# Optimization experiments

Measured on AMD Instinct MI355X. Metric: run time of the kernel, lower is better.

Reference implementation:

```python
import jax, jax.numpy as jnp
import numpy as np

B = 128        # graphs
NPG = 64       # nodes per graph (num_node)
N = B * NPG    # total nodes = 8192
IN = 16        # in_channels
D = 128        # d_model
OUT = 64       # out_channels
CAT = IN * NPG + NPG * NPG  # 5120
EPS = 1e-5


def _lin_init(k, fi, fo):
    s = 1.0 / np.sqrt(fi)
    kw, kb = jax.random.split(k)
    W = jax.random.uniform(kw, (fi, fo), jnp.float32, -s, s)
    b = jax.random.uniform(kb, (fo,), jnp.float32, -s, s)
    return W, b


def setup_inputs() -> dict:
    key = jax.random.key(0)
    ks = jax.random.split(key, 10)
    x = jax.random.normal(ks[0], (N, IN), jnp.float32)
    # complete graph (all i->j pairs, incl. self loops) per graph, offset per graph
    ii = np.repeat(np.arange(NPG), NPG)
    jj = np.tile(np.arange(NPG), NPG)
    off = (np.arange(B) * NPG)[:, None]
    row = (ii[None, :] + off).reshape(-1)
    col = (jj[None, :] + off).reshape(-1)
    edge_index = jnp.asarray(np.stack([row, col]), jnp.int32)  # [2, E]
    E = edge_index.shape[1]
    edge_weight = jax.random.uniform(ks[1], (E,), jnp.float32)
    batch = jnp.repeat(jnp.arange(B, dtype=jnp.int32), NPG)
    W1, b1 = _lin_init(ks[2], IN, D)
    W2, b2 = _lin_init(ks[3], D, D)
    Wm0, bm0 = _lin_init(ks[4], D + CAT, D)
    Wm1, bm1 = _lin_init(ks[5], D, D)
    Wm2, bm2 = _lin_init(ks[6], D, D)
    Wout, bout = _lin_init(ks[7], D, OUT)
    ones = jnp.ones((D,), jnp.float32)
    zeros = jnp.zeros((D,), jnp.float32)
    return dict(x=x, edge_index=edge_index, edge_weight=edge_weight, batch=batch,
                W1=W1, b1=b1, W2=W2, b2=b2,
                Wm0=Wm0, bm0=bm0, g0=ones, be0=zeros,
                Wm1=Wm1, bm1=bm1, g1=ones, be1=zeros,
                Wm2=Wm2, bm2=bm2, g2=ones, be2=zeros,
                Wout=Wout, bout=bout)


def _gcn_conv(h_in, row, col, ew, W, b):
    # PyG GCNConv: linear first, then D^-1/2 (A) D^-1/2 aggregation (self loops already present)
    h = h_in @ W                                             # [N, F]
    deg = jax.ops.segment_sum(ew, col, num_segments=N)       # in-degree by edge weight
    dinv = jnp.where(deg > 0, jax.lax.rsqrt(deg), 0.0)
    norm = dinv[row] * ew * dinv[col]                        # [E]
    out = jax.ops.segment_sum(norm[:, None] * h[row], col, num_segments=N)
    return out + b


def _bn(h, g, b):
    # BatchNorm1d, training-mode math (biased variance), eps=1e-5
    m = jnp.mean(h, axis=0)
    v = jnp.var(h, axis=0)
    return g * (h - m) * jax.lax.rsqrt(v + EPS) + b


def reference(x, edge_index, edge_weight, batch,
              W1, b1, W2, b2,
              Wm0, bm0, g0, be0,
              Wm1, bm1, g1, be1,
              Wm2, bm2, g2, be2,
              Wout, bout):
    row, col = edge_index[0], edge_index[1]
    h = _gcn_conv(x, row, col, edge_weight, W1, b1)
    h = jax.nn.relu(h)
    h = _gcn_conv(h, row, col, edge_weight, W2, b2)
    # global_mean_pool
    sums = jax.ops.segment_sum(h, batch, num_segments=B)
    cnt = jax.ops.segment_sum(jnp.ones((N,), h.dtype), batch, num_segments=B)
    pooled = sums / cnt[:, None]
    pooled = jax.nn.relu(pooled)
    feat = jnp.concatenate([pooled, x.reshape(B, -1), edge_weight.reshape(B, -1)], axis=1)
    feat = jax.nn.relu(feat)
    h = _bn(jax.nn.relu(feat @ Wm0 + bm0), g0, be0)
    h = _bn(jax.nn.relu(h @ Wm1 + bm1), g1, be1)
    h = _bn(jax.nn.relu(h @ Wm2 + bm2), g2, be2)
    return h @ Wout + bout
```

## Files before the change

kernel.cpp:

```cpp
#include <hip/hip_runtime.h>

#define NG 128
#define NPG 64
#define IN 16
#define DM 128
#define NOUT 64
#define EPG 4096
#define NCH 128
#define BN_EPS 1e-5f

__global__ __launch_bounds__(256) void k_front(
    const float* __restrict__ x, const float* __restrict__ ew,
    const float* __restrict__ W1, const float* __restrict__ b1,
    const float* __restrict__ W2, const float* __restrict__ b2,
    const float* __restrict__ Wm0,
    float* __restrict__ part, float* __restrict__ ppart,
    float* __restrict__ stats)
{
    __shared__ __align__(16) float u[16128];
    const int bid = blockIdx.x, t = threadIdx.x;

    if (bid < 128) {
        float* ew_s     = u;
        float* x_s      = u + 4096;
        float* W1_s     = u + 5120;
        float* P_s      = u + 7168;
        float* b1_s     = u + 15360;
        float* dinv_s   = u + 15488;
        float* t_s      = u + 15552;
        float* zp       = u + 4096;
        float* z_full   = u + 15616;
        float* pooled_s = u + 15744;
        float* pp2      = u + 15872;
        const int g = bid;
        if (bid == 0) {
            for (int i = t; i < 768; i += 256) stats[i] = 0.f;
        }
        {
            const float4* ew4 = (const float4*)(ew + g * EPG);
            float4* ews4 = (float4*)ew_s;
            #pragma unroll
            for (int i = 0; i < 4; i++) ews4[t + 256 * i] = ew4[t + 256 * i];
            const int xi = t & 63, k4 = (t >> 6) * 4;
            float4 xv = *(const float4*)(x + g * NPG * IN + xi * IN + k4);
            x_s[(k4 + 0) * 64 + xi] = xv.x;
            x_s[(k4 + 1) * 64 + xi] = xv.y;
            x_s[(k4 + 2) * 64 + xi] = xv.z;
            x_s[(k4 + 3) * 64 + xi] = xv.w;
            ((float4*)W1_s)[t]       = ((const float4*)W1)[t];
            ((float4*)W1_s)[t + 256] = ((const float4*)W1)[t + 256];
            if (t < 128) b1_s[t] = b1[t];
        }
        __syncthreads();

        if (t < NPG) {
            float s = 0.f;
            #pragma unroll 8
            for (int i = 0; i < NPG; i++) s += ew_s[i * NPG + t];
            dinv_s[t] = (s > 0.f) ? rsqrtf(s) : 0.f;
        }
        __syncthreads();

        {
            const int j = t & 63, q = t >> 6;
            const float dj = dinv_s[j];
            for (int i = q * 16; i < q * 16 + 16; i++) {
                float vv = ew_s[i * NPG + j] * dj;
                #pragma unroll
                for (int off = 32; off > 0; off >>= 1) vv += __shfl_down(vv, off, 64);
                if (j == 0) t_s[i] = dinv_s[i] * vv * (1.f / 64.f);
            }
        }

        {
            const int it = t & 15, ft = t >> 4;
            const int i0 = it * 4, f0 = ft * 8;
            float accp[4][8];
            #pragma unroll
            for (int a = 0; a < 4; a++)
                #pragma unroll
                for (int c = 0; c < 8; c++) accp[a][c] = 0.f;
            #pragma unroll
            for (int k = 0; k < IN; k++) {
                const float4 a4  = *(const float4*)(x_s + k * 64 + i0);
                const float4 b0v = *(const float4*)(W1_s + k * DM + f0);
                const float4 b1v = *(const float4*)(W1_s + k * DM + f0 + 4);
                const float av[4] = {a4.x, a4.y, a4.z, a4.w};
                const float bv[8] = {b0v.x, b0v.y, b0v.z, b0v.w, b1v.x, b1v.y, b1v.z, b1v.w};
                #pragma unroll
                for (int a = 0; a < 4; a++)
                    #pragma unroll
                    for (int c = 0; c < 8; c++) accp[a][c] += av[a] * bv[c];
            }
            #pragma unroll
            for (int a = 0; a < 4; a++) {
                const float di = dinv_s[i0 + a];
                float4* o = (float4*)(P_s + (i0 + a) * DM + f0);
                o[0] = make_float4(di * accp[a][0], di * accp[a][1],
                                   di * accp[a][2], di * accp[a][3]);
                o[1] = make_float4(di * accp[a][4], di * accp[a][5],
                                   di * accp[a][6], di * accp[a][7]);
            }
        }
        __syncthreads();

        {
            const int jt = t & 15, ft = t >> 4;
            const int j0 = jt * 4, f0 = ft * 8;
            float acc[4][8];
            #pragma unroll
            for (int a = 0; a < 4; a++)
                #pragma unroll
                for (int c = 0; c < 8; c++) acc[a][c] = 0.f;
            #pragma unroll 4
            for (int k = 0; k < 64; k++) {
                const float4 a4  = *(const float4*)(ew_s + k * 64 + j0);
                const float4 b0v = *(const float4*)(P_s + k * DM + f0);
                const float4 b1v = *(const float4*)(P_s + k * DM + f0 + 4);
                const float av[4] = {a4.x, a4.y, a4.z, a4.w};
                const float bv[8] = {b0v.x, b0v.y, b0v.z, b0v.w, b1v.x, b1v.y, b1v.z, b1v.w};
                #pragma unroll
                for (int a = 0; a < 4; a++)
                    #pragma unroll
                    for (int c = 0; c < 8; c++) acc[a][c] += av[a] * bv[c];
            }
            float zpart[8];
            #pragma unroll
            for (int c = 0; c < 8; c++) zpart[c] = 0.f;
            #pragma unroll
            for (int a = 0; a < 4; a++) {
                const float dj = dinv_s[j0 + a], tj = t_s[j0 + a];
                #pragma unroll
                for (int c = 0; c < 8; c++) {
                    float h = fmaxf(dj * acc[a][c] + b1_s[f0 + c], 0.f);
                    zpart[c] += tj * h;
                }
            }
            float4* zo = (float4*)(zp + jt * 132 + f0);
            zo[0] = make_float4(zpart[0], zpart[1], zpart[2], zpart[3]);
            zo[1] = make_float4(zpart[4], zpart[5], zpart[6], zpart[7]);
        }
        __syncthreads();

        if (t < 128) {
            float s = 0.f;
            #pragma unroll
            for (int jt = 0; jt < 16; jt++) s += zp[jt * 132 + t];
            z_full[t] = s;
        }
        __syncthreads();

        {
            const int c = t & 127, kh = t >> 7;
            float acc = 0.f;
            #pragma unroll 8
            for (int k = kh * 64; k < kh * 64 + 64; k++)
                acc += z_full[k] * W2[k * DM + c];
            pp2[kh * 128 + c] = acc;
        }
        __syncthreads();
        if (t < 128) pooled_s[t] = fmaxf(pp2[t] + pp2[128 + t] + b2[t], 0.f);
        __syncthreads();

        {
            const int f = t & 127, kh = t >> 7;
            float acc = 0.f;
            #pragma unroll 8
            for (int k = kh * 64; k < kh * 64 + 64; k++)
                acc += pooled_s[k] * Wm0[k * DM + f];
            pp2[kh * 128 + f] = acc;
        }
        __syncthreads();
        if (t < 128) ppart[g * DM + t] = pp2[t] + pp2[128 + t];
    } else {
        const int c = bid - 128;
        const int kc = c >> 1, fh = c & 1;
        const int K0 = kc * 80;
        float* a_s = u;
        float* b_s = u + 10560;

        #pragma unroll 4
        for (int it = 0; it < 32; it++) {
            int idx = it * 256 + t;
            int gg = idx >> 6, k = idx & 63;
            int K = K0 + k;
            float val = (K < 1024) ? x[gg * 1024 + K] : ew[gg * 4096 + (K - 1024)];
            a_s[k * 132 + gg] = fmaxf(val, 0.f);
        }
        #pragma unroll 4
        for (int it = 0; it < 8; it++) {
            int idx = it * 256 + t;
            int gg = idx >> 4, k = 64 + (idx & 15);
            int K = K0 + k;
            float val = (K < 1024) ? x[gg * 1024 + K] : ew[gg * 4096 + (K - 1024)];
            a_s[k * 132 + gg] = fmaxf(val, 0.f);
        }
        #pragma unroll 4
        for (int it = 0; it < 20; it++) {
            int idx = it * 256 + t;
            int k = idx >> 6, fl = idx & 63;
            b_s[k * 64 + fl] = Wm0[(128 + K0 + k) * 128 + fh * 64 + fl];
        }
        __syncthreads();

        const int gthr = t & 31, fthr = t >> 5;
        const int g0 = gthr * 4, f0 = fthr * 8;
        float acc[4][8];
        #pragma unroll
        for (int i = 0; i < 4; i++)
            #pragma unroll
            for (int jx = 0; jx < 8; jx++) acc[i][jx] = 0.f;

        #pragma unroll 4
        for (int k = 0; k < 80; k++) {
            const float4 a4  = *(const float4*)(a_s + k * 132 + g0);
            const float4 c0v = *(const float4*)(b_s + k * 64 + f0);
            const float4 c1v = *(const float4*)(b_s + k * 64 + f0 + 4);
            const float av[4] = {a4.x, a4.y, a4.z, a4.w};
            const float bv[8] = {c0v.x, c0v.y, c0v.z, c0v.w, c1v.x, c1v.y, c1v.z, c1v.w};
            #pragma unroll
            for (int i = 0; i < 4; i++)
                #pragma unroll
                for (int jx = 0; jx < 8; jx++) acc[i][jx] += av[i] * bv[jx];
        }

        float* pp = part + (size_t)c * 8192;
        #pragma unroll
        for (int i = 0; i < 4; i++) {
            float4* o = (float4*)(pp + (g0 + i) * 64 + f0);
            o[0] = make_float4(acc[i][0], acc[i][1], acc[i][2], acc[i][3]);
            o[1] = make_float4(acc[i][4], acc[i][5], acc[i][6], acc[i][7]);
        }
    }
}

__global__ __launch_bounds__(256) void k_reduce_bn0(
    const float* __restrict__ part, const float* __restrict__ ppart,
    const float* __restrict__ bm0, float* __restrict__ v0,
    float* __restrict__ stats0)
{
    __shared__ float r1[1024];
    __shared__ float sv[64], sv2[64];
    const int bx = blockIdx.x, t = threadIdx.x;
    const int fgrp = bx & 7, gt = bx >> 3;
    const int f4 = t & 3, gl = (t >> 2) & 3, ch = t >> 4;
    const int g = gt * 4 + gl;
    const int fbase = fgrp * 16 + f4 * 4;
    const int fh = fbase >> 6, fl = fbase & 63;

    const float4* p = (const float4*)part
                    + ((size_t)(2 * (ch * 4) + fh) * 8192 + g * 64 + fl) / 4;
    float4 v = make_float4(0.f, 0.f, 0.f, 0.f);
    #pragma unroll
    for (int cc = 0; cc < 4; cc++) {
        float4 x4 = p[(size_t)cc * 4096];
        v.x += x4.x; v.y += x4.y; v.z += x4.z; v.w += x4.w;
    }
    float* r = r1 + ch * 64 + gl * 16 + f4 * 4;
    r[0] = v.x; r[1] = v.y; r[2] = v.z; r[3] = v.w;
    __syncthreads();

    if (t < 64) {
        const int fsub = t & 15, gl2 = t >> 4;
        const int f = fgrp * 16 + fsub, gg = gt * 4 + gl2;
        float s = bm0[f] + ppart[gg * DM + f];
        #pragma unroll
        for (int c2 = 0; c2 < 16; c2++) s += r1[c2 * 64 + gl2 * 16 + fsub];
        s = fmaxf(s, 0.f);
        v0[gg * DM + f] = s;
        sv[t] = s; sv2[t] = s * s;
    }
    __syncthreads();
    if (t < 16) {
        float s1 = sv[t] + sv[t + 16] + sv[t + 32] + sv[t + 48];
        float s2 = sv2[t] + sv2[t + 16] + sv2[t + 32] + sv2[t + 48];
        atomicAdd(&stats0[(fgrp * 16 + t) * 2], s1);
        atomicAdd(&stats0[(fgrp * 16 + t) * 2 + 1], s2);
    }
}

__global__ __launch_bounds__(256) void k_mlp(
    const float* __restrict__ vin, const float* __restrict__ statsin,
    const float* __restrict__ gbn, const float* __restrict__ bbn,
    const float* __restrict__ W, const float* __restrict__ bias,
    float* __restrict__ vout, float* __restrict__ statsout)
{
    __shared__ float scale_s[128], shift_s[128];
    __shared__ float wcol[128];
    __shared__ float pc[256];
    __shared__ float h_s[64 * 129];
    const int b = blockIdx.x, t = threadIdx.x;
    const int f = b & 127, gh = b >> 7;
    if (t < 128) {
        float s1 = statsin[t * 2], s2 = statsin[t * 2 + 1];
        float m = s1 * (1.f / 128.f);
        float var = s2 * (1.f / 128.f) - m * m;
        float sc = gbn[t] * rsqrtf(var + BN_EPS);
        scale_s[t] = sc;
        shift_s[t] = bbn[t] - m * sc;
        wcol[t] = W[t * 128 + f];
    }
    __syncthreads();
    const int g0r = gh * 64;
    const float4* vin4 = (const float4*)(vin + g0r * 128);
    #pragma unroll
    for (int it = 0; it < 8; ++it) {
        int idx = it * 256 + t;
        int gl = idx >> 5, k4 = (idx & 31) * 4;
        float4 vv = vin4[idx];
        float* hp = h_s + gl * 129 + k4;
        hp[0] = vv.x * scale_s[k4 + 0] + shift_s[k4 + 0];
        hp[1] = vv.y * scale_s[k4 + 1] + shift_s[k4 + 1];
        hp[2] = vv.z * scale_s[k4 + 2] + shift_s[k4 + 2];
        hp[3] = vv.w * scale_s[k4 + 3] + shift_s[k4 + 3];
    }
    __syncthreads();
    {
        const int gl = t & 63, kh = t >> 6;
        float acc = 0.f;
        #pragma unroll 8
        for (int k = kh * 32; k < kh * 32 + 32; ++k) acc += h_s[gl * 129 + k] * wcol[k];
        pc[gl * 4 + kh] = acc;
    }
    __syncthreads();
    if (t < 64) {
        float v = fmaxf(pc[t * 4] + pc[t * 4 + 1] + pc[t * 4 + 2] + pc[t * 4 + 3]
                        + bias[f], 0.f);
        vout[(size_t)(g0r + t) * 128 + f] = v;
        float s1 = v, s2 = v * v;
        #pragma unroll
        for (int off = 32; off > 0; off >>= 1) {
            s1 += __shfl_down(s1, off, 64);
            s2 += __shfl_down(s2, off, 64);
        }
        if (t == 0) {
            atomicAdd(&statsout[f * 2], s1);
            atomicAdd(&statsout[f * 2 + 1], s2);
        }
    }
}

__global__ __launch_bounds__(128) void k_out(
    const float* __restrict__ vin, const float* __restrict__ statsin,
    const float* __restrict__ gbn, const float* __restrict__ bbn,
    const float* __restrict__ Wo, const float* __restrict__ bo,
    float* __restrict__ out)
{
    __shared__ __align__(16) float Wo_s[128 * 64];
    __shared__ float vrow[2][128];
    __shared__ float scale_s[128], shift_s[128];
    const int b = blockIdx.x, t = threadIdx.x, g0 = b * 2;
    {
        float s1 = statsin[t * 2], s2 = statsin[t * 2 + 1];
        float m = s1 * (1.f / 128.f);
        float var = s2 * (1.f / 128.f) - m * m;
        float sc = gbn[t] * rsqrtf(var + BN_EPS);
        scale_s[t] = sc;
        shift_s[t] = bbn[t] - m * sc;
    }
    __syncthreads();
    {
        const float4* wo4 = (const float4*)Wo;
        float4* wos4 = (float4*)Wo_s;
        #pragma unroll
        for (int it = 0; it < 16; it++) wos4[it * 128 + t] = wo4[it * 128 + t];
    }
    if (t < 64) {
        int g2 = t >> 5, k4 = (t & 31) * 4;
        float4 vv = ((const float4*)(vin + g0 * 128))[t];
        vrow[g2][k4 + 0] = vv.x * scale_s[k4 + 0] + shift_s[k4 + 0];
        vrow[g2][k4 + 1] = vv.y * scale_s[k4 + 1] + shift_s[k4 + 1];
        vrow[g2][k4 + 2] = vv.z * scale_s[k4 + 2] + shift_s[k4 + 2];
        vrow[g2][k4 + 3] = vv.w * scale_s[k4 + 3] + shift_s[k4 + 3];
    }
    __syncthreads();
    const int g2 = t >> 6, o = t & 63;
    float acc = bo[o];
    #pragma unroll 8
    for (int k = 0; k < 128; k++) acc += vrow[g2][k] * Wo_s[k * 64 + o];
    out[(g0 + g2) * NOUT + o] = acc;
}

extern "C" void kernel_launch(void* const* d_in, const int* in_sizes, int n_in,
                              void* d_out, int out_size, void* d_ws, size_t ws_size,
                              hipStream_t stream)
{
    const float* x   = (const float*)d_in[0];
    const float* ew  = (const float*)d_in[2];
    const float* W1  = (const float*)d_in[4];
    const float* b1  = (const float*)d_in[5];
    const float* W2  = (const float*)d_in[6];
    const float* b2  = (const float*)d_in[7];
    const float* Wm0 = (const float*)d_in[8];
    const float* bm0 = (const float*)d_in[9];
    const float* g0  = (const float*)d_in[10];
    const float* be0 = (const float*)d_in[11];
    const float* Wm1 = (const float*)d_in[12];
    const float* bm1 = (const float*)d_in[13];
    const float* g1  = (const float*)d_in[14];
    const float* be1 = (const float*)d_in[15];
    const float* Wm2 = (const float*)d_in[16];
    const float* bm2 = (const float*)d_in[17];
    const float* g2  = (const float*)d_in[18];
    const float* be2 = (const float*)d_in[19];
    const float* Wo  = (const float*)d_in[20];
    const float* bo  = (const float*)d_in[21];

    float* ws     = (float*)d_ws;
    float* part   = ws;
    float* ppartb = part + NCH * 8192;
    float* v0     = ppartb + 16384;
    float* v1     = v0 + 16384;
    float* v2     = v1 + 16384;
    float* stats  = v2 + 16384;

    k_front<<<256, 256, 0, stream>>>(x, ew, W1, b1, W2, b2, Wm0, part, ppartb, stats);
    k_reduce_bn0<<<256, 256, 0, stream>>>(part, ppartb, bm0, v0, stats);
    k_mlp<<<256, 256, 0, stream>>>(v0, stats,       g0, be0, Wm1, bm1, v1, stats + 256);
    k_mlp<<<256, 256, 0, stream>>>(v1, stats + 256, g1, be1, Wm2, bm2, v2, stats + 512);
    k_out<<<NOUT, 128, 0, stream>>>(v2, stats + 512, g2, be2, Wo, bo, (float*)d_out);
}
```

Measured before the change: 132.8 us.

## Fuse all stages into one persistent kernel with atomic grid barriers

Merges the front, reduction/BN0, two MLP layers and output projection into a single 256-block kernel separated by software grid barriers built on atomic counters. A memset clears the barrier counters and stats, replacing the in-kernel zeroing. The aim is to remove four kernel launch gaps and tail effects. It also vectorizes the A/B tile loads in the Wm0 partial-GEMM blocks to float4, issuing all loads before the shared-memory stores. The barrier relies on all 256 blocks being co-resident and adds spin-wait cost at each phase.

New measurement: 191.1 us. 1.44x slower.

```diff
diff --git a/kernel.cpp b/kernel.cpp
--- a/kernel.cpp
+++ b/kernel.cpp
@@ -1,23 +1,106 @@
 #include <hip/hip_runtime.h>
 
-#define NG 128
 #define NPG 64
 #define IN 16
 #define DM 128
 #define NOUT 64
 #define EPG 4096
-#define NCH 128
 #define BN_EPS 1e-5f
 
-__global__ __launch_bounds__(256) void k_front(
+__device__ __forceinline__ void gbar(unsigned* ctr) {
+    __syncthreads();
+    if (threadIdx.x == 0) {
+        __threadfence();
+        atomicAdd(ctr, 1u);
+        while (atomicAdd(ctr, 0u) < 256u) __builtin_amdgcn_s_sleep(2);
+        __threadfence();
+    }
+    __syncthreads();
+}
+
+__device__ void mlp_phase(float* u,
+    const float* __restrict__ vin, const float* __restrict__ statsin,
+    const float* __restrict__ gbn, const float* __restrict__ bbn,
+    const float* __restrict__ W, const float* __restrict__ bias,
+    float* __restrict__ vout, float* __restrict__ statsout)
+{
+    float* scale_s = u;
+    float* shift_s = u + 128;
+    float* wcol    = u + 256;
+    float* pc      = u + 384;
+    float* h_s     = u + 640;
+    const int b = blockIdx.x, t = threadIdx.x;
+    const int f = b & 127, gh = b >> 7;
+    if (t < 128) {
+        float s1 = statsin[t * 2], s2 = statsin[t * 2 + 1];
+        float m = s1 * (1.f / 128.f);
+        float var = s2 * (1.f / 128.f) - m * m;
+        float sc = gbn[t] * rsqrtf(var + BN_EPS);
+        scale_s[t] = sc;
+        shift_s[t] = bbn[t] - m * sc;
+        wcol[t] = W[t * 128 + f];
+    }
+    __syncthreads();
+    const int g0r = gh * 64;
+    const float4* vin4 = (const float4*)(vin + g0r * 128);
+    #pragma unroll
+    for (int it = 0; it < 8; ++it) {
+        int idx = it * 256 + t;
+        int gl = idx >> 5, k4 = (idx & 31) * 4;
+        float4 vv = vin4[idx];
+        float* hp = h_s + gl * 129 + k4;
+        hp[0] = vv.x * scale_s[k4 + 0] + shift_s[k4 + 0];
+        hp[1] = vv.y * scale_s[k4 + 1] + shift_s[k4 + 1];
+        hp[2] = vv.z * scale_s[k4 + 2] + shift_s[k4 + 2];
+        hp[3] = vv.w * scale_s[k4 + 3] + shift_s[k4 + 3];
+    }
+    __syncthreads();
+    {
+        const int gl = t & 63, kh = t >> 6;
+        float acc = 0.f;
+        #pragma unroll 8
+        for (int k = kh * 32; k < kh * 32 + 32; ++k) acc += h_s[gl * 129 + k] * wcol[k];
+        pc[gl * 4 + kh] = acc;
+    }
+    __syncthreads();
+    if (t < 64) {
+        float v = fmaxf(pc[t * 4] + pc[t * 4 + 1] + pc[t * 4 + 2] + pc[t * 4 + 3]
+                        + bias[f], 0.f);
+        vout[(size_t)(g0r + t) * 128 + f] = v;
+        float s1 = v, s2 = v * v;
+        #pragma unroll
+        for (int off = 32; off > 0; off >>= 1) {
+            s1 += __shfl_down(s1, off, 64);
+            s2 += __shfl_down(s2, off, 64);
+        }
+        if (t == 0) {
+            atomicAdd(&statsout[f * 2], s1);
+            atomicAdd(&statsout[f * 2 + 1], s2);
+        }
+    }
+}
+
+__global__ __launch_bounds__(256) void k_fused(
     const float* __restrict__ x, const float* __restrict__ ew,
     const float* __restrict__ W1, const float* __restrict__ b1,
     const float* __restrict__ W2, const float* __restrict__ b2,
-    const float* __restrict__ Wm0,
-    float* __restrict__ part, float* __restrict__ ppart,
-    float* __restrict__ stats)
+    const float* __restrict__ Wm0, const float* __restrict__ bm0,
+    const float* __restrict__ gbn0, const float* __restrict__ bbn0,
+    const float* __restrict__ Wm1, const float* __restrict__ bm1,
+    const float* __restrict__ gbn1, const float* __restrict__ bbn1,
+    const float* __restrict__ Wm2, const float* __restrict__ bm2,
+    const float* __restrict__ gbn2, const float* __restrict__ bbn2,
+    const float* __restrict__ Wo, const float* __restrict__ bo,
+    float* __restrict__ ws, float* __restrict__ out)
 {
     __shared__ __align__(16) float u[16128];
+    unsigned* bar = (unsigned*)ws;
+    float* stats = ws + 256;
+    float* part  = ws + 1024;
+    float* ppart = part + 128 * 8192;
+    float* v0 = ppart + 16384;
+    float* v1 = v0 + 16384;
+    float* v2 = v1 + 16384;
     const int bid = blockIdx.x, t = threadIdx.x;
 
     if (bid < 128) {
@@ -33,9 +116,6 @@
         float* pooled_s = u + 15744;
         float* pp2      = u + 15872;
         const int g = bid;
-        if (bid == 0) {
-            for (int i = t; i < 768; i += 256) stats[i] = 0.f;
-        }
         {
             const float4* ew4 = (const float4*)(ew + g * EPG);
             float4* ews4 = (float4*)ew_s;
@@ -179,27 +259,54 @@
         float* a_s = u;
         float* b_s = u + 10560;
 
-        #pragma unroll 4
-        for (int it = 0; it < 32; it++) {
-            int idx = it * 256 + t;
-            int gg = idx >> 6, k = idx & 63;
-            int K = K0 + k;
-            float val = (K < 1024) ? x[gg * 1024 + K] : ew[gg * 4096 + (K - 1024)];
-            a_s[k * 132 + gg] = fmaxf(val, 0.f);
-        }
-        #pragma unroll 4
+        float4 va[8], vb2[2], vc[5];
+        #pragma unroll
         for (int it = 0; it < 8; it++) {
             int idx = it * 256 + t;
-            int gg = idx >> 4, k = 64 + (idx & 15);
-            int K = K0 + k;
-            float val = (K < 1024) ? x[gg * 1024 + K] : ew[gg * 4096 + (K - 1024)];
-            a_s[k * 132 + gg] = fmaxf(val, 0.f);
-        }
-        #pragma unroll 4
-        for (int it = 0; it < 20; it++) {
-            int idx = it * 256 + t;
-            int k = idx >> 6, fl = idx & 63;
-            b_s[k * 64 + fl] = Wm0[(128 + K0 + k) * 128 + fh * 64 + fl];
+            int gg = idx >> 4, k4 = (idx & 15) << 2;
+            int K = K0 + k4;
+            const float* src = (K < 1024) ? (x + gg * 1024 + K)
+                                          : (ew + gg * 4096 + (K - 1024));
+            va[it] = *(const float4*)src;
+        }
+        #pragma unroll
+        for (int it = 0; it < 2; it++) {
+            int idx = it * 256 + t;
+            int gg = idx >> 2, k4 = 64 + ((idx & 3) << 2);
+            int K = K0 + k4;
+            const float* src = (K < 1024) ? (x + gg * 1024 + K)
+                                          : (ew + gg * 4096 + (K - 1024));
+            vb2[it] = *(const float4*)src;
+        }
+        #pragma unroll
+        for (int it = 0; it < 5; it++) {
+            int idx = it * 256 + t;
+            int k = idx >> 4, fl4 = (idx & 15) << 2;
+            vc[it] = *(const float4*)(Wm0 + (size_t)(128 + K0 + k) * 128 + fh * 64 + fl4);
+        }
+        #pragma unroll
+        for (int it = 0; it < 8; it++) {
+            int idx = it * 256 + t;
+            int gg = idx >> 4, k4 = (idx & 15) << 2;
+            a_s[(k4 + 0) * 132 + gg] = fmaxf(va[it].x, 0.f);
+            a_s[(k4 + 1) * 132 + gg] = fmaxf(va[it].y, 0.f);
+            a_s[(k4 + 2) * 132 + gg] = fmaxf(va[it].z, 0.f);
+            a_s[(k4 + 3) * 132 + gg] = fmaxf(va[it].w, 0.f);
+        }
+        #pragma unroll
+        for (int it = 0; it < 2; it++) {
+            int idx = it * 256 + t;
+            int gg = idx >> 2, k4 = 64 + ((idx & 3) << 2);
+            a_s[(k4 + 0) * 132 + gg] = fmaxf(vb2[it].x, 0.f);
+            a_s[(k4 + 1) * 132 + gg] = fmaxf(vb2[it].y, 0.f);
+            a_s[(k4 + 2) * 132 + gg] = fmaxf(vb2[it].z, 0.f);
+            a_s[(k4 + 3) * 132 + gg] = fmaxf(vb2[it].w, 0.f);
+        }
+        #pragma unroll
+        for (int it = 0; it < 5; it++) {
+            int idx = it * 256 + t;
+            int k = idx >> 4, fl4 = (idx & 15) << 2;
+            *(float4*)(b_s + k * 64 + fl4) = vc[it];
         }
         __syncthreads();
 
@@ -232,153 +339,91 @@
             o[1] = make_float4(acc[i][4], acc[i][5], acc[i][6], acc[i][7]);
         }
     }
-}
-
-__global__ __launch_bounds__(256) void k_reduce_bn0(
-    const float* __restrict__ part, const float* __restrict__ ppart,
-    const float* __restrict__ bm0, float* __restrict__ v0,
-    float* __restrict__ stats0)
-{
-    __shared__ float r1[1024];
-    __shared__ float sv[64], sv2[64];
-    const int bx = blockIdx.x, t = threadIdx.x;
-    const int fgrp = bx & 7, gt = bx >> 3;
-    const int f4 = t & 3, gl = (t >> 2) & 3, ch = t >> 4;
-    const int g = gt * 4 + gl;
-    const int fbase = fgrp * 16 + f4 * 4;
-    const int fh = fbase >> 6, fl = fbase & 63;
-
-    const float4* p = (const float4*)part
-                    + ((size_t)(2 * (ch * 4) + fh) * 8192 + g * 64 + fl) / 4;
-    float4 v = make_float4(0.f, 0.f, 0.f, 0.f);
-    #pragma unroll
-    for (int cc = 0; cc < 4; cc++) {
-        float4 x4 = p[(size_t)cc * 4096];
-        v.x += x4.x; v.y += x4.y; v.z += x4.z; v.w += x4.w;
-    }
-    float* r = r1 + ch * 64 + gl * 16 + f4 * 4;
-    r[0] = v.x; r[1] = v.y; r[2] = v.z; r[3] = v.w;
-    __syncthreads();
-
-    if (t < 64) {
-        const int fsub = t & 15, gl2 = t >> 4;
-        const int f = fgrp * 16 + fsub, gg = gt * 4 + gl2;
-        float s = bm0[f] + ppart[gg * DM + f];
-        #pragma unroll
-        for (int c2 = 0; c2 < 16; c2++) s += r1[c2 * 64 + gl2 * 16 + fsub];
-        s = fmaxf(s, 0.f);
-        v0[gg * DM + f] = s;
-        sv[t] = s; sv2[t] = s * s;
-    }
-    __syncthreads();
-    if (t < 16) {
-        float s1 = sv[t] + sv[t + 16] + sv[t + 32] + sv[t + 48];
-        float s2 = sv2[t] + sv2[t + 16] + sv2[t + 32] + sv2[t + 48];
-        atomicAdd(&stats0[(fgrp * 16 + t) * 2], s1);
-        atomicAdd(&stats0[(fgrp * 16 + t) * 2 + 1], s2);
-    }
-}
-
-__global__ __launch_bounds__(256) void k_mlp(
-    const float* __restrict__ vin, const float* __restrict__ statsin,
-    const float* __restrict__ gbn, const float* __restrict__ bbn,
-    const float* __restrict__ W, const float* __restrict__ bias,
-    float* __restrict__ vout, float* __restrict__ statsout)
-{
-    __shared__ float scale_s[128], shift_s[128];
-    __shared__ float wcol[128];
-    __shared__ float pc[256];
-    __shared__ float h_s[64 * 129];
-    const int b = blockIdx.x, t = threadIdx.x;
-    const int f = b & 127, gh = b >> 7;
-    if (t < 128) {
-        float s1 = statsin[t * 2], s2 = statsin[t * 2 + 1];
-        float m = s1 * (1.f / 128.f);
-        float var = s2 * (1.f / 128.f) - m * m;
-        float sc = gbn[t] * rsqrtf(var + BN_EPS);
-        scale_s[t] = sc;
-        shift_s[t] = bbn[t] - m * sc;
-        wcol[t] = W[t * 128 + f];
-    }
-    __syncthreads();
-    const int g0r = gh * 64;
-    const float4* vin4 = (const float4*)(vin + g0r * 128);
-    #pragma unroll
-    for (int it = 0; it < 8; ++it) {
-        int idx = it * 256 + t;
-        int gl = idx >> 5, k4 = (idx & 31) * 4;
-        float4 vv = vin4[idx];
-        float* hp = h_s + gl * 129 + k4;
-        hp[0] = vv.x * scale_s[k4 + 0] + shift_s[k4 + 0];
-        hp[1] = vv.y * scale_s[k4 + 1] + shift_s[k4 + 1];
-        hp[2] = vv.z * scale_s[k4 + 2] + shift_s[k4 + 2];
-        hp[3] = vv.w * scale_s[k4 + 3] + shift_s[k4 + 3];
-    }
-    __syncthreads();
+    gbar(bar + 0);
+
     {
-        const int gl = t & 63, kh = t >> 6;
-        float acc = 0.f;
+        float* r1  = u;
+        float* sv  = u + 1024;
+        float* sv2 = u + 1088;
+        const int fgrp = bid & 7, gt = bid >> 3;
+        const int f4 = t & 3, gl = (t >> 2) & 3, ch = t >> 4;
+        const int g = gt * 4 + gl;
+        const int fbase = fgrp * 16 + f4 * 4;
+        const int fh = fbase >> 6, fl = fbase & 63;
+        const float4* p = (const float4*)part
+                        + ((size_t)(2 * (ch * 4) + fh) * 8192 + g * 64 + fl) / 4;
+        float4 v = make_float4(0.f, 0.f, 0.f, 0.f);
+        #pragma unroll
+        for (int cc = 0; cc < 4; cc++) {
+            float4 x4 = p[(size_t)cc * 4096];
+            v.x += x4.x; v.y += x4.y; v.z += x4.z; v.w += x4.w;
+        }
+        float* r = r1 + ch * 64 + gl * 16 + f4 * 4;
+        r[0] = v.x; r[1] = v.y; r[2] = v.z; r[3] = v.w;
+        __syncthreads();
+
+        if (t < 64) {
+            const int fsub = t & 15, gl2 = t >> 4;
+            const int f = fgrp * 16 + fsub, gg = gt * 4 + gl2;
+            float s = bm0[f] + ppart[gg * DM + f];
+            #pragma unroll
+            for (int c2 = 0; c2 < 16; c2++) s += r1[c2 * 64 + gl2 * 16 + fsub];
+            s = fmaxf(s, 0.f);
+            v0[gg * DM + f] = s;
+            sv[t] = s; sv2[t] = s * s;
+        }
+        __syncthreads();
+        if (t < 16) {
+            float s1 = sv[t] + sv[t + 16] + sv[t + 32] + sv[t + 48];
+            float s2 = sv2[t] + sv2[t + 16] + sv2[t + 32] + sv2[t + 48];
+            atomicAdd(&stats[(fgrp * 16 + t) * 2], s1);
+            atomicAdd(&stats[(fgrp * 16 + t) * 2 + 1], s2);
+        }
+    }
+    gbar(bar + 16);
+
+    mlp_phase(u, v0, stats,       gbn0, bbn0, Wm1, bm1, v1, stats + 256);
+    gbar(bar + 32);
+    mlp_phase(u, v1, stats + 256, gbn1, bbn1, Wm2, bm2, v2, stats + 512);
+    gbar(bar + 48);
+
+    if (bid < 32) {
+        float* Wo_s    = u;
+        float* vrow    = u + 8192;
+        float* scale_s = u + 8704;
+        float* shift_s = u + 8832;
+        const float* st2 = stats + 512;
+        const int gq = bid * 4;
+        if (t < 128) {
+            float s1 = st2[t * 2], s2 = st2[t * 2 + 1];
+            float m = s1 * (1.f / 128.f);
+            float var = s2 * (1.f / 128.f) - m * m;
+            float sc = gbn2[t] * rsqrtf(var + BN_EPS);
+            scale_s[t] = sc;
+            shift_s[t] = bbn2[t] - m * sc;
+        }
+        __syncthreads();
+        {
+            const float4* wo4 = (const float4*)Wo;
+            float4* wos4 = (float4*)Wo_s;
+            #pragma unroll
+            for (int it = 0; it < 8; it++) wos4[it * 256 + t] = wo4[it * 256 + t];
+        }
+        if (t < 128) {
+            const int r = t >> 5, k4 = (t & 31) * 4;
+            float4 vv = ((const float4*)(v2 + gq * 128))[t];
+            vrow[r * 128 + k4 + 0] = vv.x * scale_s[k4 + 0] + shift_s[k4 + 0];
+            vrow[r * 128 + k4 + 1] = vv.y * scale_s[k4 + 1] + shift_s[k4 + 1];
+            vrow[r * 128 + k4 + 2] = vv.z * scale_s[k4 + 2] + shift_s[k4 + 2];
+            vrow[r * 128 + k4 + 3] = vv.w * scale_s[k4 + 3] + shift_s[k4 + 3];
+        }
+        __syncthreads();
+        const int g2 = t >> 6, o = t & 63;
+        float acc = bo[o];
         #pragma unroll 8
-        for (int k = kh * 32; k < kh * 32 + 32; ++k) acc += h_s[gl * 129 + k] * wcol[k];
-        pc[gl * 4 + kh] = acc;
-    }
-    __syncthreads();
-    if (t < 64) {
-        float v = fmaxf(pc[t * 4] + pc[t * 4 + 1] + pc[t * 4 + 2] + pc[t * 4 + 3]
-                        + bias[f], 0.f);
-        vout[(size_t)(g0r + t) * 128 + f] = v;
-        float s1 = v, s2 = v * v;
-        #pragma unroll
-        for (int off = 32; off > 0; off >>= 1) {
-            s1 += __shfl_down(s1, off, 64);
-            s2 += __shfl_down(s2, off, 64);
-        }
-        if (t == 0) {
-            atomicAdd(&statsout[f * 2], s1);
-            atomicAdd(&statsout[f * 2 + 1], s2);
-        }
-    }
-}
-
-__global__ __launch_bounds__(128) void k_out(
-    const float* __restrict__ vin, const float* __restrict__ statsin,
-    const float* __restrict__ gbn, const float* __restrict__ bbn,
-    const float* __restrict__ Wo, const float* __restrict__ bo,
-    float* __restrict__ out)
-{
-    __shared__ __align__(16) float Wo_s[128 * 64];
-    __shared__ float vrow[2][128];
-    __shared__ float scale_s[128], shift_s[128];
-    const int b = blockIdx.x, t = threadIdx.x, g0 = b * 2;
-    {
-        float s1 = statsin[t * 2], s2 = statsin[t * 2 + 1];
-        float m = s1 * (1.f / 128.f);
-        float var = s2 * (1.f / 128.f) - m * m;
-        float sc = gbn[t] * rsqrtf(var + BN_EPS);
-        scale_s[t] = sc;
-        shift_s[t] = bbn[t] - m * sc;
-    }
-    __syncthreads();
-    {
-        const float4* wo4 = (const float4*)Wo;
-        float4* wos4 = (float4*)Wo_s;
-        #pragma unroll
-        for (int it = 0; it < 16; it++) wos4[it * 128 + t] = wo4[it * 128 + t];
-    }
-    if (t < 64) {
-        int g2 = t >> 5, k4 = (t & 31) * 4;
-        float4 vv = ((const float4*)(vin + g0 * 128))[t];
-        vrow[g2][k4 + 0] = vv.x * scale_s[k4 + 0] + shift_s[k4 + 0];
-        vrow[g2][k4 + 1] = vv.y * scale_s[k4 + 1] + shift_s[k4 + 1];
-        vrow[g2][k4 + 2] = vv.z * scale_s[k4 + 2] + shift_s[k4 + 2];
-        vrow[g2][k4 + 3] = vv.w * scale_s[k4 + 3] + shift_s[k4 + 3];
-    }
-    __syncthreads();
-    const int g2 = t >> 6, o = t & 63;
-    float acc = bo[o];
-    #pragma unroll 8
-    for (int k = 0; k < 128; k++) acc += vrow[g2][k] * Wo_s[k * 64 + o];
-    out[(g0 + g2) * NOUT + o] = acc;
+        for (int k = 0; k < 128; k++) acc += vrow[g2 * 128 + k] * Wo_s[k * 64 + o];
+        out[(gq + g2) * NOUT + o] = acc;
+    }
 }
 
 extern "C" void kernel_launch(void* const* d_in, const int* in_sizes, int n_in,
@@ -406,17 +451,11 @@
     const float* Wo  = (const float*)d_in[20];
     const float* bo  = (const float*)d_in[21];
 
-    float* ws     = (float*)d_ws;
-    float* part   = ws;
-    float* ppartb = part + NCH * 8192;
-    float* v0     = ppartb + 16384;
-    float* v1     = v0 + 16384;
-    float* v2     = v1 + 16384;
-    float* stats  = v2 + 16384;
-
-    k_front<<<256, 256, 0, stream>>>(x, ew, W1, b1, W2, b2, Wm0, part, ppartb, stats);
-    k_reduce_bn0<<<256, 256, 0, stream>>>(part, ppartb, bm0, v0, stats);
-    k_mlp<<<256, 256, 0, stream>>>(v0, stats,       g0, be0, Wm1, bm1, v1, stats + 256);
-    k_mlp<<<256, 256, 0, stream>>>(v1, stats + 256, g1, be1, Wm2, bm2, v2, stats + 512);
-    k_out<<<NOUT, 128, 0, stream>>>(v2, stats + 512, g2, be2, Wo, bo, (float*)d_out);
+    float* ws = (float*)d_ws;
+    hipMemsetAsync(d_ws, 0, 4096, stream);
+    k_fused<<<256, 256, 0, stream>>>(x, ew, W1, b1, W2, b2,
+                                     Wm0, bm0, g0, be0,
+                                     Wm1, bm1, g1, be1,
+                                     Wm2, bm2, g2, be2,
+                                     Wo, bo, ws, (float*)d_out);
 }
```
